# Kernel tuning notes

Hardware: AMD Instinct MI355X
Metric: run time of the kernel (lower is better)

The kernel has to match this reference:

```python
import jax, jax.numpy as jnp
import numpy as np

NUM_GRIDS = 8
GRID = jnp.linspace(-2.0, 2.0, NUM_GRIDS)
DENOM = 4.0 / (NUM_GRIDS - 1)
H, D = 8, 64
Q_DIM = K_DIM = V_DIM = 512
TOT = H * D


def fastkan(x, ln_s, ln_b, sw, bw, bb):
    # LayerNorm over last dim
    mu = jnp.mean(x, axis=-1, keepdims=True)
    var = jnp.var(x, axis=-1, keepdims=True)
    xn = (x - mu) * jax.lax.rsqrt(var + 1e-5) * ln_s + ln_b
    # Gaussian RBF basis over fixed grid: [..., in, G]
    basis = jnp.exp(-jnp.square((xn[..., None] - GRID) / DENOM))
    flat = basis.reshape(*x.shape[:-1], x.shape[-1] * NUM_GRIDS)
    # spline linear + base update (silu -> linear)
    return flat @ sw.T + jax.nn.silu(x) @ bw.T + bb


def setup_inputs() -> dict:
    key = jax.random.key(0)
    keys = iter(jax.random.split(key, 32))
    B, QL, KL = 2, 2048, 2048
    inp = {
        "q": jax.random.normal(next(keys), (B, QL, Q_DIM), jnp.float32),
        "k": jax.random.normal(next(keys), (B, KL, K_DIM), jnp.float32),
        "v": jax.random.normal(next(keys), (B, KL, V_DIM), jnp.float32),
    }
    def layer(ind, outd):
        return {
            "ln_s": jnp.ones((ind,), jnp.float32),
            "ln_b": jnp.zeros((ind,), jnp.float32),
            "sw": jax.random.normal(next(keys), (outd, ind * NUM_GRIDS), jnp.float32) * (0.1 / np.sqrt(ind * NUM_GRIDS)),
            "bw": jax.random.normal(next(keys), (outd, ind), jnp.float32) / np.sqrt(ind),
            "bb": jnp.zeros((outd,), jnp.float32),
        }
    dims = {"lq": (Q_DIM, TOT), "lk": (K_DIM, TOT), "lv": (V_DIM, TOT), "lo": (TOT, Q_DIM), "lg": (Q_DIM, TOT)}
    for name, (i, o) in dims.items():
        for pn, arr in layer(i, o).items():
            inp[name + "_" + pn] = arr
    return inp


def reference(q, k, v,
              lq_ln_s, lq_ln_b, lq_sw, lq_bw, lq_bb,
              lk_ln_s, lk_ln_b, lk_sw, lk_bw, lk_bb,
              lv_ln_s, lv_ln_b, lv_sw, lv_bw, lv_bb,
              lo_ln_s, lo_ln_b, lo_sw, lo_bw, lo_bb,
              lg_ln_s, lg_ln_b, lg_sw, lg_bw, lg_bb):
    norm = D ** -0.5
    wq = fastkan(q, lq_ln_s, lq_ln_b, lq_sw, lq_bw, lq_bb).reshape(*q.shape[:-1], H, D) * norm
    wk = fastkan(k, lk_ln_s, lk_ln_b, lk_sw, lk_bw, lk_bb).reshape(*k.shape[:-1], H, D)
    # att: [b, q_len, k_len, h]; softmax over k_len (axis=-2), matching torch code
    att = jax.nn.softmax(jnp.einsum('bqhd,bkhd->bqkh', wq, wk), axis=-2)
    wv = fastkan(v, lv_ln_s, lv_ln_b, lv_sw, lv_bw, lv_bb).reshape(*v.shape[:-1], H, D)
    o = jnp.einsum('bqkh,bkhd->bqhd', att, wv).reshape(*q.shape[:-1], TOT)
    g = fastkan(q, lg_ln_s, lg_ln_b, lg_sw, lg_bw, lg_bb)
    o = jax.nn.sigmoid(g) * o
    return fastkan(o, lo_ln_s, lo_ln_b, lo_sw, lo_bw, lo_bb)
```

## Files before the change

### kernel.cpp

```cpp
#include <hip/hip_runtime.h>

typedef unsigned short u16;
typedef unsigned int u32;
typedef float f32x4 __attribute__((ext_vector_type(4)));
typedef short s16x8 __attribute__((ext_vector_type(8)));

#define IND 512
#define KSPL 4096
#define NOUT 512
#define MROWS 4096
#define LQ 2048
#define AST 72
#define NZ 8
#define NSPLIT 4

#define SWN (4096 * 512)
#define BWN (512 * 512)
#define LSTR ((size_t)(SWN + BWN + 512))

__device__ __forceinline__ float bf2f(u16 u) {
    union { u32 i; float f; } v; v.i = ((u32)u) << 16; return v.f;
}
__device__ __forceinline__ u16 f2bf(float f) {
    union { float f; u32 i; } v; v.f = f;
    u32 x = v.i;
    return (u16)((x + 0x7FFFu + ((x >> 16) & 1u)) >> 16);
}
__device__ __forceinline__ uint4 pack8(float4 a, float4 b) {
    uint4 p;
    p.x = (u32)f2bf(a.x) | ((u32)f2bf(a.y) << 16);
    p.y = (u32)f2bf(a.z) | ((u32)f2bf(a.w) << 16);
    p.z = (u32)f2bf(b.x) | ((u32)f2bf(b.y) << 16);
    p.w = (u32)f2bf(b.z) | ((u32)f2bf(b.w) << 16);
    return p;
}
__device__ __forceinline__ void gl_lds16(const u16* g, u16* l) {
    __builtin_amdgcn_global_load_lds((const __attribute__((address_space(1))) void*)g,
                                     (__attribute__((address_space(3))) void*)l, 16, 0, 0);
}

__global__ void detect_dtype(const u32* __restrict__ qraw, u32* __restrict__ flag)
{
    const int t = threadIdx.x;
    int cnt = 0;
    for (int i = t; i < 1024; i += 256) {
        u32 e = (qraw[i] >> 23) & 0xFFu;
        if (e >= 100u && e <= 140u) cnt++;
    }
    #pragma unroll
    for (int off = 32; off > 0; off >>= 1) cnt += __shfl_down(cnt, off);
    __shared__ int red[4];
    if ((t & 63) == 0) red[t >> 6] = cnt;
    __syncthreads();
    if (t == 0) flag[0] = (red[0] + red[1] + red[2] + red[3] > 512) ? 1u : 0u;
}

struct WSrc { const void* p[15]; };
__global__ __launch_bounds__(256) void convert_w(WSrc s, u16* __restrict__ wb, const u32* __restrict__ flag)
{
    const int r = blockIdx.y;
    const int l = r / 3, t = r - l * 3;
    const int n = (t == 0) ? SWN : ((t == 1) ? BWN : 512);
    const int i = (blockIdx.x * 256 + threadIdx.x) * 8;
    if (i >= n) return;
    u16* dst = wb + (size_t)l * LSTR + ((t == 0) ? 0 : ((t == 1) ? SWN : SWN + BWN)) + i;
    const void* src = s.p[r];
    if (flag[0]) {
        const float* f = (const float*)src;
        *(uint4*)dst = pack8(*(const float4*)&f[i], *(const float4*)&f[i + 4]);
    } else {
        *(uint4*)dst = *(const uint4*)&((const u16*)src)[i];
    }
}

__global__ __launch_bounds__(256) void prep_kan(
    const void* __restrict__ xv, const void* __restrict__ ln_sv, const void* __restrict__ ln_bv,
    u16* __restrict__ basis, u16* __restrict__ silu, const u32* __restrict__ flag)
{
    const int row = blockIdx.x;
    const int t = threadIdx.x;
    const bool isf = flag[0] != 0u;
    float x0, x1;
    if (isf) {
        const float* xr = (const float*)xv + (size_t)row * IND;
        x0 = xr[t]; x1 = xr[t + 256];
    } else {
        const u16* xr = (const u16*)xv + (size_t)row * IND;
        x0 = bf2f(xr[t]); x1 = bf2f(xr[t + 256]);
    }
    float s = x0 + x1;
    float ss = x0 * x0 + x1 * x1;
    #pragma unroll
    for (int off = 32; off > 0; off >>= 1) {
        s += __shfl_down(s, off);
        ss += __shfl_down(ss, off);
    }
    __shared__ float red[8];
    const int wid = t >> 6, ln = t & 63;
    if (ln == 0) { red[wid] = s; red[4 + wid] = ss; }
    __syncthreads();
    const float tot = red[0] + red[1] + red[2] + red[3];
    const float tot2 = red[4] + red[5] + red[6] + red[7];
    const float mu = tot * (1.0f / IND);
    const float rstd = rsqrtf(tot2 * (1.0f / IND) - mu * mu + 1e-5f);
    #pragma unroll
    for (int e = 0; e < 2; e++) {
        const int i = t + e * 256;
        const float xi = (e == 0) ? x0 : x1;
        float lns, lnb;
        if (isf) {
            lns = ((const float*)ln_sv)[i];
            lnb = ((const float*)ln_bv)[i];
        } else {
            lns = bf2f(((const u16*)ln_sv)[i]);
            lnb = bf2f(((const u16*)ln_bv)[i]);
        }
        const float xn = (xi - mu) * rstd * lns + lnb;
        u16 o8[8];
        #pragma unroll
        for (int g = 0; g < 8; g++) {
            float d = (xn - (-2.0f + g * (4.0f / 7.0f))) * 1.75f;
            o8[g] = f2bf(__expf(-d * d));
        }
        uint4 pk;
        pk.x = (u32)o8[0] | ((u32)o8[1] << 16);
        pk.y = (u32)o8[2] | ((u32)o8[3] << 16);
        pk.z = (u32)o8[4] | ((u32)o8[5] << 16);
        pk.w = (u32)o8[6] | ((u32)o8[7] << 16);
        *(uint4*)(basis + (size_t)row * KSPL + i * 8) = pk;
        silu[(size_t)row * IND + i] = f2bf(xi / (1.0f + __expf(-xi)));
    }
}

__global__ __launch_bounds__(256) void prep_merge(
    const float* __restrict__ Opart, const float* __restrict__ lpart,
    const u16* __restrict__ gbuf, const void* __restrict__ ln_sv, const void* __restrict__ ln_bv,
    u16* __restrict__ basis, u16* __restrict__ silu, const u32* __restrict__ flag)
{
    const int row = blockIdx.x;
    const int b = row >> 11, qr = row & (LQ - 1);
    const int t = threadIdx.x;
    const bool isf = flag[0] != 0u;

    float xv[2];
    #pragma unroll
    for (int e = 0; e < 2; e++) {
        const int col = t + e * 256;
        const int g = b * 8 + (col >> 6);
        const int dd = col & 63;
        float o = 0.0f, l = 0.0f;
        #pragma unroll
        for (int s = 0; s < NSPLIT; s++) {
            const size_t rb = ((size_t)s * 16 + g) * LQ + qr;
            o += Opart[rb * 64 + dd];
            l += lpart[rb];
        }
        const float gv = bf2f(gbuf[(size_t)row * IND + col]);
        xv[e] = (o / l) / (1.0f + __expf(-gv));
    }
    float s = xv[0] + xv[1];
    float ss = xv[0] * xv[0] + xv[1] * xv[1];
    #pragma unroll
    for (int off = 32; off > 0; off >>= 1) {
        s += __shfl_down(s, off);
        ss += __shfl_down(ss, off);
    }
    __shared__ float red[8];
    const int wid = t >> 6, ln = t & 63;
    if (ln == 0) { red[wid] = s; red[4 + wid] = ss; }
    __syncthreads();
    const float tot = red[0] + red[1] + red[2] + red[3];
    const float tot2 = red[4] + red[5] + red[6] + red[7];
    const float mu = tot * (1.0f / IND);
    const float rstd = rsqrtf(tot2 * (1.0f / IND) - mu * mu + 1e-5f);
    #pragma unroll
    for (int e = 0; e < 2; e++) {
        const int i = t + e * 256;
        const float xi = xv[e];
        float lns, lnb;
        if (isf) {
            lns = ((const float*)ln_sv)[i];
            lnb = ((const float*)ln_bv)[i];
        } else {
            lns = bf2f(((const u16*)ln_sv)[i]);
            lnb = bf2f(((const u16*)ln_bv)[i]);
        }
        const float xn = (xi - mu) * rstd * lns + lnb;
        u16 o8[8];
        #pragma unroll
        for (int g = 0; g < 8; g++) {
            float d = (xn - (-2.0f + g * (4.0f / 7.0f))) * 1.75f;
            o8[g] = f2bf(__expf(-d * d));
        }
        uint4 pk;
        pk.x = (u32)o8[0] | ((u32)o8[1] << 16);
        pk.y = (u32)o8[2] | ((u32)o8[3] << 16);
        pk.z = (u32)o8[4] | ((u32)o8[5] << 16);
        pk.w = (u32)o8[6] | ((u32)o8[7] << 16);
        *(uint4*)(basis + (size_t)row * KSPL + i * 8) = pk;
        silu[(size_t)row * IND + i] = f2bf(xi / (1.0f + __expf(-xi)));
    }
}

__global__ __launch_bounds__(512) void gemm_big(
    const u16* __restrict__ A1, const u16* __restrict__ B1,
    const u16* __restrict__ A2, const u16* __restrict__ B2,
    u16* __restrict__ P)
{
    __shared__ __align__(16) u16 sA[2][256 * 64];
    __shared__ __align__(16) u16 sB[2][256 * 64];
    const int tid = threadIdx.x;
    const int lane = tid & 63;
    const int wid = tid >> 6;
    const int fm = lane & 15;
    const int quad = lane >> 4;
    const int wmbase = (wid >> 2) * 128;
    const int wnbase = (wid & 3) * 64;
    const int mbase = blockIdx.x * 256;
    const int nbase = blockIdx.y * 256;
    const int kz = blockIdx.z;

    const int srow = wid * 8 + (lane >> 3);
    const int scol = ((lane & 7) ^ (lane >> 3)) * 8;
    const int k1b = kz * 512;
    const int k2b = kz * 64;

    f32x4 acc[8][4] = {};

    {
        const u16* b0 = B1 + (size_t)(nbase + srow) * KSPL + k1b + scol;
        const u16* a0 = A1 + (size_t)(mbase + srow) * KSPL + k1b + scol;
        #pragma unroll
        for (int i = 0; i < 4; i++) gl_lds16(b0 + (size_t)i * 64 * KSPL, &sB[0][i * 4096 + wid * 512]);
        #pragma unroll
        for (int i = 0; i < 4; i++) gl_lds16(a0 + (size_t)i * 64 * KSPL, &sA[0][i * 4096 + wid * 512]);
        #pragma unroll
        for (int i = 0; i < 4; i++) gl_lds16(b0 + 64 + (size_t)i * 64 * KSPL, &sB[1][i * 4096 + wid * 512]);
    }
    asm volatile("s_waitcnt vmcnt(4)" ::: "memory");
    asm volatile("s_barrier" ::: "memory");

    #pragma unroll 1
    for (int t = 0; t < 9; ++t) {
        const u16* Ac = &sA[t & 1][0];
        const u16* Bc = &sB[t & 1][0];
        u16* abuf = &sA[(t + 1) & 1][0];
        u16* bbuf = &sB[t & 1][0];

        const u16* aS = nullptr; const u16* bS = nullptr;
        size_t aStep = 0, bStep = 0;
        if (t + 1 < 8) {
            aS = A1 + (size_t)(mbase + srow) * KSPL + k1b + (t + 1) * 64 + scol;
            aStep = (size_t)64 * KSPL;
        } else if (t + 1 == 8) {
            aS = A2 + (size_t)(mbase + srow) * IND + k2b + scol;
            aStep = (size_t)64 * IND;
        }
        if (t + 2 < 8) {
            bS = B1 + (size_t)(nbase + srow) * KSPL + k1b + (t + 2) * 64 + scol;
            bStep = (size_t)64 * KSPL;
        } else if (t + 2 == 8) {
            bS = B2 + (size_t)(nbase + srow) * IND + k2b + scol;
            bStep = (size_t)64 * IND;
        }

        s16x8 bfrag[4][2];
        #pragma unroll
        for (int n = 0; n < 4; n++)
            #pragma unroll
            for (int ks = 0; ks < 2; ks++)
                bfrag[n][ks] = *(const s16x8*)&Bc[((wnbase + n * 16 + fm) << 6) +
                                                 ((((ks << 2) + quad) ^ (fm & 7)) << 3)];

        #pragma unroll
        for (int ph = 0; ph < 2; ++ph) {
            s16x8 afr[4][2];
            #pragma unroll
            for (int i = 0; i < 4; i++)
                #pragma unroll
                for (int ks = 0; ks < 2; ks++)
                    afr[i][ks] = *(const s16x8*)&Ac[((wmbase + (ph * 4 + i) * 16 + fm) << 6) +
                                                   ((((ks << 2) + quad) ^ (fm & 7)) << 3)];
            if (ph == 0) {
                if (aS) {
                    #pragma unroll
                    for (int i = 0; i < 4; i++)
                        gl_lds16(aS + (size_t)i * aStep, abuf + i * 4096 + wid * 512);
                }
            } else {
                if (bS) {
                    #pragma unroll
                    for (int i = 0; i < 4; i++)
                        gl_lds16(bS + (size_t)i * bStep, bbuf + i * 4096 + wid * 512);
                }
            }
            asm volatile("s_barrier" ::: "memory");
            __builtin_amdgcn_s_setprio(1);
            #pragma unroll
            for (int i = 0; i < 4; i++)
                #pragma unroll
                for (int n = 0; n < 4; n++) {
                    acc[ph * 4 + i][n] = __builtin_amdgcn_mfma_f32_16x16x32_bf16(afr[i][0], bfrag[n][0], acc[ph * 4 + i][n], 0, 0, 0);
                    acc[ph * 4 + i][n] = __builtin_amdgcn_mfma_f32_16x16x32_bf16(afr[i][1], bfrag[n][1], acc[ph * 4 + i][n], 0, 0, 0);
                }
            __builtin_amdgcn_s_setprio(0);
            if (ph == 1) {
                if (t < 7)       asm volatile("s_waitcnt vmcnt(4)" ::: "memory");
                else if (t == 7) asm volatile("s_waitcnt vmcnt(0)" ::: "memory");
            }
            asm volatile("s_barrier" ::: "memory");
        }
    }

    #pragma unroll
    for (int n = 0; n < 4; n++) {
        const int col = nbase + wnbase + n * 16 + fm;
        const size_t cb = ((size_t)kz * NOUT + col) * MROWS;
        #pragma unroll
        for (int m = 0; m < 8; m++) {
            const int row0 = mbase + wmbase + m * 16 + quad * 4;
            uint2 o;
            o.x = (u32)f2bf(acc[m][n][0]) | ((u32)f2bf(acc[m][n][1]) << 16);
            o.y = (u32)f2bf(acc[m][n][2]) | ((u32)f2bf(acc[m][n][3]) << 16);
            *(uint2*)&P[cb + row0] = o;
        }
    }
}

__global__ __launch_bounds__(256) void reduce_kan(
    const u16* __restrict__ P, const u16* __restrict__ bias, void* __restrict__ C,
    float scale, const u32* __restrict__ flag, int ext_out)
{
    __shared__ float tshf[64][65];
    const int row0 = blockIdx.x * 64;
    const int col0 = blockIdx.y * 64;
    const int tid = threadIdx.x;
    #pragma unroll
    for (int p = 0; p < 2; p++) {
        const int idx = tid + p * 256;
        const int cl = idx >> 3;
        const int r8 = (idx & 7) * 8;
        float a[8] = {};
        for (int kz = 0; kz < NZ; kz++) {
            uint4 pk = *(const uint4*)&P[((size_t)kz * NOUT + col0 + cl) * MROWS + row0 + r8];
            const u16* pv = (const u16*)&pk;
            #pragma unroll
            for (int u = 0; u < 8; u++) a[u] += bf2f(pv[u]);
        }
        const float bi = bf2f(bias[col0 + cl]);
        #pragma unroll
        for (int u = 0; u < 8; u++) tshf[r8 + u][cl] = (a[u] + bi) * scale;
    }
    __syncthreads();
    const bool fo = ext_out && (flag[0] != 0u);
    #pragma unroll
    for (int p = 0; p < 2; p++) {
        const int idx = tid + p * 256;
        const int rl = idx >> 3;
        const int c8 = (idx & 7) * 8;
        if (fo) {
            float* Cf = (float*)C + (size_t)(row0 + rl) * NOUT + col0 + c8;
            float4 f0, f1;
            f0.x = tshf[rl][c8 + 0]; f0.y = tshf[rl][c8 + 1];
            f0.z = tshf[rl][c8 + 2]; f0.w = tshf[rl][c8 + 3];
            f1.x = tshf[rl][c8 + 4]; f1.y = tshf[rl][c8 + 5];
            f1.z = tshf[rl][c8 + 6]; f1.w = tshf[rl][c8 + 7];
            *(float4*)Cf = f0;
            *(float4*)(Cf + 4) = f1;
        } else {
            uint4 o;
            o.x = (u32)f2bf(tshf[rl][c8 + 0]) | ((u32)f2bf(tshf[rl][c8 + 1]) << 16);
            o.y = (u32)f2bf(tshf[rl][c8 + 2]) | ((u32)f2bf(tshf[rl][c8 + 3]) << 16);
            o.z = (u32)f2bf(tshf[rl][c8 + 4]) | ((u32)f2bf(tshf[rl][c8 + 5]) << 16);
            o.w = (u32)f2bf(tshf[rl][c8 + 6]) | ((u32)f2bf(tshf[rl][c8 + 7]) << 16);
            *(uint4*)&((u16*)C)[(size_t)(row0 + rl) * NOUT + col0 + c8] = o;
        }
    }
}

__global__ __launch_bounds__(256) void reduce_vt(
    const u16* __restrict__ P, const u16* __restrict__ bias, u16* __restrict__ VT)
{
    const int bc = blockIdx.x;
    const int b = bc >> 9, col = bc & 511;
    const int row8 = threadIdx.x * 8;
    float a[8] = {};
    for (int kz = 0; kz < NZ; kz++) {
        uint4 pk = *(const uint4*)&P[((size_t)kz * NOUT + col) * MROWS + b * LQ + row8];
        const u16* pv = (const u16*)&pk;
        #pragma unroll
        for (int u = 0; u < 8; u++) a[u] += bf2f(pv[u]);
    }
    const float bi = bf2f(bias[col]);
    u16 tmp[8];
    #pragma unroll
    for (int u = 0; u < 8; u++) tmp[u] = f2bf(a[u] + bi);
    *(uint4*)&VT[(size_t)bc * LQ + row8] = *(const uint4*)tmp;
}

__global__ __launch_bounds__(256) void attn4(
    const u16* __restrict__ wqp, const u16* __restrict__ wkp, const u16* __restrict__ VT,
    float* __restrict__ Opart, float* __restrict__ lpart)
{
    __shared__ __align__(16) u16 Ks[64 * 64];
    __shared__ __align__(16) u16 Vs[64 * 64];
    __shared__ __align__(16) u16 Ps[4][32 * AST];

    const int tid = threadIdx.x;
    const int lane = tid & 63;
    const int wid = tid >> 6;
    const int quad = lane >> 4;
    const int fm = lane & 15;
    const int srow8 = lane >> 3;
    const int schk = (lane & 7) ^ (lane >> 3);
    const int qb = blockIdx.x * 128;
    const int g = blockIdx.y;
    const int s = blockIdx.z;
    const int b = g >> 3, h = g & 7;
    const size_t qkbase = ((size_t)b * LQ) * 512 + h * 64;
    const size_t vtbase = (size_t)g * 64 * LQ;
    const int kvlen = LQ / NSPLIT, kv0 = s * kvlen;

    s16x8 aq[2][2];
    #pragma unroll
    for (int qi = 0; qi < 2; qi++)
        #pragma unroll
        for (int ks = 0; ks < 2; ks++)
            aq[qi][ks] = *(const s16x8*)&wqp[qkbase +
                (size_t)(qb + wid * 32 + qi * 16 + fm) * 512 + ks * 32 + quad * 8];
    s16x8 ones;
    #pragma unroll
    for (int i = 0; i < 8; i++) ones[i] = (short)0x3F80;

    f32x4 oacc[2][4] = {};
    f32x4 lacc[2] = {};

    for (int kt = 0; kt < kvlen / 64; kt++) {
        const int kb = kv0 + kt * 64;
        #pragma unroll
        for (int gg = 0; gg < 2; gg++) {
            const int r = wid * 16 + gg * 8 + srow8;
            gl_lds16(&wkp[qkbase + (size_t)(kb + r) * 512 + schk * 8], &Ks[(wid * 16 + gg * 8) * 64]);
            gl_lds16(&VT[vtbase + (size_t)r * LQ + kb + schk * 8],     &Vs[(wid * 16 + gg * 8) * 64]);
        }
        __syncthreads();

        #pragma unroll
        for (int j = 0; j < 4; j++) {
            f32x4 z0 = {}, z1 = {};
            #pragma unroll
            for (int ks = 0; ks < 2; ks++) {
                s16x8 bk = *(const s16x8*)&Ks[((j * 16 + fm) << 6) +
                                              ((((ks << 2) + quad) ^ (fm & 7)) << 3)];
                z0 = __builtin_amdgcn_mfma_f32_16x16x32_bf16(aq[0][ks], bk, z0, 0, 0, 0);
                z1 = __builtin_amdgcn_mfma_f32_16x16x32_bf16(aq[1][ks], bk, z1, 0, 0, 0);
            }
            #pragma unroll
            for (int r = 0; r < 4; r++) {
                union { float f; u32 i; } u0, u1;
                u0.f = __expf(z0[r] - 12.0f);
                u1.f = __expf(z1[r] - 12.0f);
                Ps[wid][(quad * 4 + r) * AST + j * 16 + fm]        = (u16)(u0.i >> 16);
                Ps[wid][(16 + quad * 4 + r) * AST + j * 16 + fm]   = (u16)(u1.i >> 16);
            }
        }

        s16x8 ap[2][2];
        #pragma unroll
        for (int qi = 0; qi < 2; qi++)
            #pragma unroll
            for (int ks = 0; ks < 2; ks++)
                ap[qi][ks] = *(const s16x8*)&Ps[wid][(qi * 16 + fm) * AST + ks * 32 + quad * 8];
        #pragma unroll
        for (int jd = 0; jd < 4; jd++)
            #pragma unroll
            for (int ks = 0; ks < 2; ks++) {
                s16x8 bv = *(const s16x8*)&Vs[((jd * 16 + fm) << 6) +
                                              ((((ks << 2) + quad) ^ (fm & 7)) << 3)];
                oacc[0][jd] = __builtin_amdgcn_mfma_f32_16x16x32_bf16(ap[0][ks], bv, oacc[0][jd], 0, 0, 0);
                oacc[1][jd] = __builtin_amdgcn_mfma_f32_16x16x32_bf16(ap[1][ks], bv, oacc[1][jd], 0, 0, 0);
            }
        #pragma unroll
        for (int qi = 0; qi < 2; qi++)
            #pragma unroll
            for (int ks = 0; ks < 2; ks++)
                lacc[qi] = __builtin_amdgcn_mfma_f32_16x16x32_bf16(ap[qi][ks], ones, lacc[qi], 0, 0, 0);
        __syncthreads();
    }

    const size_t obase = ((size_t)s * 16 + g) * LQ;
    #pragma unroll
    for (int qi = 0; qi < 2; qi++) {
        #pragma unroll
        for (int jd = 0; jd < 4; jd++)
            #pragma unroll
            for (int r = 0; r < 4; r++) {
                const int qrow = qb + wid * 32 + qi * 16 + quad * 4 + r;
                Opart[(obase + qrow) * 64 + jd * 16 + fm] = oacc[qi][jd][r];
            }
        if (fm == 0) {
            #pragma unroll
            for (int r = 0; r < 4; r++) {
                const int qrow = qb + wid * 32 + qi * 16 + quad * 4 + r;
                lpart[obase + qrow] = lacc[qi][r];
            }
        }
    }
}

extern "C" void kernel_launch(void* const* d_in, const int* in_sizes, int n_in,
                              void* d_out, int out_size, void* d_ws, size_t ws_size,
                              hipStream_t stream)
{
    const void* q = d_in[0];
    const void* k = d_in[1];
    const void* v = d_in[2];
    auto P = [&](int i) { return (const void*)d_in[i]; };

    const size_t WB_BYTES  = 5 * LSTR * 2;
    const size_t BAS_BYTES = (size_t)MROWS * KSPL * 2;
    const size_t SIL_BYTES = (size_t)MROWS * IND * 2;
    const size_t PART_B    = (size_t)NZ * MROWS * NOUT * 2;
    const size_t VT_B      = (size_t)16 * 64 * LQ * 2;
    const size_t OPART_B   = (size_t)NSPLIT * 16 * LQ * 64 * 4;

    char* base = (char*)d_ws;
    u32*  flag  = (u32*)base;
    u16*  wb    = (u16*)(base + 4096);
    u16*  basis = (u16*)((char*)wb + WB_BYTES);
    u16*  silu  = (u16*)((char*)basis + BAS_BYTES);
    u16*  wq    = (u16*)((char*)silu + SIL_BYTES);
    u16*  wk    = wq + (size_t)MROWS * NOUT;
    u16*  gbuf  = wk + (size_t)MROWS * NOUT;
    u16*  part  = gbuf + (size_t)MROWS * NOUT;
    u16*  VT    = (u16*)((char*)part + PART_B);
    float* Opart = (float*)((char*)VT + VT_B);
    float* lpart = (float*)((char*)Opart + OPART_B);

    detect_dtype<<<1, 256, 0, stream>>>((const u32*)q, flag);

    WSrc srcs;
    const int lbase[5] = {3, 8, 13, 18, 23};
    for (int l = 0; l < 5; l++) {
        srcs.p[l * 3 + 0] = d_in[lbase[l] + 2];
        srcs.p[l * 3 + 1] = d_in[lbase[l] + 3];
        srcs.p[l * 3 + 2] = d_in[lbase[l] + 4];
    }
    convert_w<<<dim3(SWN / 2048, 15), 256, 0, stream>>>(srcs, wb, flag);

    auto swb = [&](int l) { return wb + (size_t)l * LSTR; };
    auto bwb = [&](int l) { return wb + (size_t)l * LSTR + SWN; };
    auto bbb = [&](int l) { return wb + (size_t)l * LSTR + SWN + BWN; };
    dim3 gg(MROWS / 256, NOUT / 256, NZ);
    dim3 rg(MROWS / 64, NOUT / 64);

    prep_kan<<<MROWS, 256, 0, stream>>>(q, P(3), P(4), basis, silu, flag);
    gemm_big<<<gg, 512, 0, stream>>>(basis, swb(0), silu, bwb(0), part);
    reduce_kan<<<rg, 256, 0, stream>>>(part, bbb(0), wq, 0.125f, flag, 0);
    prep_kan<<<MROWS, 256, 0, stream>>>(q, P(23), P(24), basis, silu, flag);
    gemm_big<<<gg, 512, 0, stream>>>(basis, swb(4), silu, bwb(4), part);
    reduce_kan<<<rg, 256, 0, stream>>>(part, bbb(4), gbuf, 1.0f, flag, 0);
    prep_kan<<<MROWS, 256, 0, stream>>>(k, P(8), P(9), basis, silu, flag);
    gemm_big<<<gg, 512, 0, stream>>>(basis, swb(1), silu, bwb(1), part);
    reduce_kan<<<rg, 256, 0, stream>>>(part, bbb(1), wk, 1.0f, flag, 0);
    prep_kan<<<MROWS, 256, 0, stream>>>(v, P(13), P(14), basis, silu, flag);
    gemm_big<<<gg, 512, 0, stream>>>(basis, swb(2), silu, bwb(2), part);
    reduce_vt<<<1024, 256, 0, stream>>>(part, bbb(2), VT);

    attn4<<<dim3(LQ / 128, 16, NSPLIT), 256, 0, stream>>>(wq, wk, VT, Opart, lpart);

    prep_merge<<<MROWS, 256, 0, stream>>>(Opart, lpart, gbuf, P(18), P(19), basis, silu, flag);
    gemm_big<<<gg, 512, 0, stream>>>(basis, swb(3), silu, bwb(3), part);
    reduce_kan<<<rg, 256, 0, stream>>>(part, bbb(3), d_out, 1.0f, flag, 1);
}
```

Measured before the change: 421.4 us.

## Replace double-buffered 256x256 GEMM tile with simple single-buffered 128x128 tile

The KAN GEMM kernel shrinks from a 256x256 output tile with 512 threads and a hand-scheduled double-buffered LDS pipeline to a 128x128 tile with 256 threads. The new kernel loads each K chunk, syncs, computes, and syncs again, with no prefetch overlap. This gives four times as many blocks and less LDS per block, which may let more blocks share a CU. The cost is losing the load/compute overlap, the priority hints, and data reuse from the larger tile.

```diff
diff --git a/kernel.cpp b/kernel.cpp
--- a/kernel.cpp
+++ b/kernel.cpp
@@ -202,126 +202,80 @@
     }
 }
 
-__global__ __launch_bounds__(512) void gemm_big(
+__global__ __launch_bounds__(256) void gemm_big(
     const u16* __restrict__ A1, const u16* __restrict__ B1,
     const u16* __restrict__ A2, const u16* __restrict__ B2,
     u16* __restrict__ P)
 {
-    __shared__ __align__(16) u16 sA[2][256 * 64];
-    __shared__ __align__(16) u16 sB[2][256 * 64];
+    __shared__ __align__(16) u16 sA[128 * 64];
+    __shared__ __align__(16) u16 sB[128 * 64];
     const int tid = threadIdx.x;
     const int lane = tid & 63;
     const int wid = tid >> 6;
     const int fm = lane & 15;
     const int quad = lane >> 4;
-    const int wmbase = (wid >> 2) * 128;
-    const int wnbase = (wid & 3) * 64;
-    const int mbase = blockIdx.x * 256;
-    const int nbase = blockIdx.y * 256;
+    const int wm = (wid >> 1) * 64;
+    const int wn = (wid & 1) * 64;
+    const int mbase = blockIdx.x * 128;
+    const int nbase = blockIdx.y * 128;
     const int kz = blockIdx.z;
 
     const int srow = wid * 8 + (lane >> 3);
     const int scol = ((lane & 7) ^ (lane >> 3)) * 8;
-    const int k1b = kz * 512;
-    const int k2b = kz * 64;
-
-    f32x4 acc[8][4] = {};
-
-    {
-        const u16* b0 = B1 + (size_t)(nbase + srow) * KSPL + k1b + scol;
-        const u16* a0 = A1 + (size_t)(mbase + srow) * KSPL + k1b + scol;
-        #pragma unroll
-        for (int i = 0; i < 4; i++) gl_lds16(b0 + (size_t)i * 64 * KSPL, &sB[0][i * 4096 + wid * 512]);
-        #pragma unroll
-        for (int i = 0; i < 4; i++) gl_lds16(a0 + (size_t)i * 64 * KSPL, &sA[0][i * 4096 + wid * 512]);
-        #pragma unroll
-        for (int i = 0; i < 4; i++) gl_lds16(b0 + 64 + (size_t)i * 64 * KSPL, &sB[1][i * 4096 + wid * 512]);
-    }
-    asm volatile("s_waitcnt vmcnt(4)" ::: "memory");
-    asm volatile("s_barrier" ::: "memory");
+
+    f32x4 acc[4][4] = {};
+
+    const u16* aP  = A1 + (size_t)(mbase + srow) * KSPL + kz * 512 + scol;
+    const u16* bP  = B1 + (size_t)(nbase + srow) * KSPL + kz * 512 + scol;
+    const u16* aP2 = A2 + (size_t)(mbase + srow) * IND + kz * 64 + scol;
+    const u16* bP2 = B2 + (size_t)(nbase + srow) * IND + kz * 64 + scol;
 
     #pragma unroll 1
     for (int t = 0; t < 9; ++t) {
-        const u16* Ac = &sA[t & 1][0];
-        const u16* Bc = &sB[t & 1][0];
-        u16* abuf = &sA[(t + 1) & 1][0];
-        u16* bbuf = &sB[t & 1][0];
-
-        const u16* aS = nullptr; const u16* bS = nullptr;
-        size_t aStep = 0, bStep = 0;
-        if (t + 1 < 8) {
-            aS = A1 + (size_t)(mbase + srow) * KSPL + k1b + (t + 1) * 64 + scol;
-            aStep = (size_t)64 * KSPL;
-        } else if (t + 1 == 8) {
-            aS = A2 + (size_t)(mbase + srow) * IND + k2b + scol;
-            aStep = (size_t)64 * IND;
-        }
-        if (t + 2 < 8) {
-            bS = B1 + (size_t)(nbase + srow) * KSPL + k1b + (t + 2) * 64 + scol;
-            bStep = (size_t)64 * KSPL;
-        } else if (t + 2 == 8) {
-            bS = B2 + (size_t)(nbase + srow) * IND + k2b + scol;
-            bStep = (size_t)64 * IND;
-        }
-
-        s16x8 bfrag[4][2];
-        #pragma unroll
-        for (int n = 0; n < 4; n++)
-            #pragma unroll
-            for (int ks = 0; ks < 2; ks++)
-                bfrag[n][ks] = *(const s16x8*)&Bc[((wnbase + n * 16 + fm) << 6) +
-                                                 ((((ks << 2) + quad) ^ (fm & 7)) << 3)];
-
-        #pragma unroll
-        for (int ph = 0; ph < 2; ++ph) {
-            s16x8 afr[4][2];
-            #pragma unroll
-            for (int i = 0; i < 4; i++)
-                #pragma unroll
-                for (int ks = 0; ks < 2; ks++)
-                    afr[i][ks] = *(const s16x8*)&Ac[((wmbase + (ph * 4 + i) * 16 + fm) << 6) +
-                                                   ((((ks << 2) + quad) ^ (fm & 7)) << 3)];
-            if (ph == 0) {
-                if (aS) {
-                    #pragma unroll
-                    for (int i = 0; i < 4; i++)
-                        gl_lds16(aS + (size_t)i * aStep, abuf + i * 4096 + wid * 512);
-                }
-            } else {
-                if (bS) {
-                    #pragma unroll
-                    for (int i = 0; i < 4; i++)
-                        gl_lds16(bS + (size_t)i * bStep, bbuf + i * 4096 + wid * 512);
-                }
-            }
-            asm volatile("s_barrier" ::: "memory");
-            __builtin_amdgcn_s_setprio(1);
-            #pragma unroll
-            for (int i = 0; i < 4; i++)
-                #pragma unroll
-                for (int n = 0; n < 4; n++) {
-                    acc[ph * 4 + i][n] = __builtin_amdgcn_mfma_f32_16x16x32_bf16(afr[i][0], bfrag[n][0], acc[ph * 4 + i][n], 0, 0, 0);
-                    acc[ph * 4 + i][n] = __builtin_amdgcn_mfma_f32_16x16x32_bf16(afr[i][1], bfrag[n][1], acc[ph * 4 + i][n], 0, 0, 0);
-                }
-            __builtin_amdgcn_s_setprio(0);
-            if (ph == 1) {
-                if (t < 7)       asm volatile("s_waitcnt vmcnt(4)" ::: "memory");
-                else if (t == 7) asm volatile("s_waitcnt vmcnt(0)" ::: "memory");
-            }
-            asm volatile("s_barrier" ::: "memory");
-        }
-    }
-
-    #pragma unroll
-    for (int n = 0; n < 4; n++) {
-        const int col = nbase + wnbase + n * 16 + fm;
+        if (t < 8) {
+            #pragma unroll
+            for (int i = 0; i < 4; i++) {
+                gl_lds16(aP + (size_t)i * 32 * KSPL + t * 64, &sA[i * 2048 + wid * 512]);
+                gl_lds16(bP + (size_t)i * 32 * KSPL + t * 64, &sB[i * 2048 + wid * 512]);
+            }
+        } else {
+            #pragma unroll
+            for (int i = 0; i < 4; i++) {
+                gl_lds16(aP2 + (size_t)i * 32 * IND, &sA[i * 2048 + wid * 512]);
+                gl_lds16(bP2 + (size_t)i * 32 * IND, &sB[i * 2048 + wid * 512]);
+            }
+        }
+        __syncthreads();
+        s16x8 af[4][2], bfr[4][2];
+        #pragma unroll
+        for (int i = 0; i < 4; i++)
+            #pragma unroll
+            for (int ks = 0; ks < 2; ks++) {
+                af[i][ks]  = *(const s16x8*)&sA[((wm + i * 16 + fm) << 6) +
+                                                ((((ks << 2) + quad) ^ (fm & 7)) << 3)];
+                bfr[i][ks] = *(const s16x8*)&sB[((wn + i * 16 + fm) << 6) +
+                                                ((((ks << 2) + quad) ^ (fm & 7)) << 3)];
+            }
+        #pragma unroll
+        for (int i = 0; i < 4; i++)
+            #pragma unroll
+            for (int j = 0; j < 4; j++) {
+                acc[i][j] = __builtin_amdgcn_mfma_f32_16x16x32_bf16(af[i][0], bfr[j][0], acc[i][j], 0, 0, 0);
+                acc[i][j] = __builtin_amdgcn_mfma_f32_16x16x32_bf16(af[i][1], bfr[j][1], acc[i][j], 0, 0, 0);
+            }
+        __syncthreads();
+    }
+
+    #pragma unroll
+    for (int j = 0; j < 4; j++) {
+        const int col = nbase + wn + j * 16 + fm;
         const size_t cb = ((size_t)kz * NOUT + col) * MROWS;
         #pragma unroll
-        for (int m = 0; m < 8; m++) {
-            const int row0 = mbase + wmbase + m * 16 + quad * 4;
+        for (int i = 0; i < 4; i++) {
+            const int row0 = mbase + wm + i * 16 + quad * 4;
             uint2 o;
-            o.x = (u32)f2bf(acc[m][n][0]) | ((u32)f2bf(acc[m][n][1]) << 16);
-            o.y = (u32)f2bf(acc[m][n][2]) | ((u32)f2bf(acc[m][n][3]) << 16);
+            o.x = (u32)f2bf(acc[i][j][0]) | ((u32)f2bf(acc[i][j][1]) << 16);
+            o.y = (u32)f2bf(acc[i][j][2]) | ((u32)f2bf(acc[i][j][3]) << 16);
             *(uint2*)&P[cb + row0] = o;
         }
     }
@@ -551,25 +505,25 @@
     auto swb = [&](int l) { return wb + (size_t)l * LSTR; };
     auto bwb = [&](int l) { return wb + (size_t)l * LSTR + SWN; };
     auto bbb = [&](int l) { return wb + (size_t)l * LSTR + SWN + BWN; };
-    dim3 gg(MROWS / 256, NOUT / 256, NZ);
+    dim3 gg(MROWS / 128, NOUT / 128, NZ);
     dim3 rg(MROWS / 64, NOUT / 64);
 
     prep_kan<<<MROWS, 256, 0, stream>>>(q, P(3), P(4), basis, silu, flag);
-    gemm_big<<<gg, 512, 0, stream>>>(basis, swb(0), silu, bwb(0), part);
+    gemm_big<<<gg, 256, 0, stream>>>(basis, swb(0), silu, bwb(0), part);
     reduce_kan<<<rg, 256, 0, stream>>>(part, bbb(0), wq, 0.125f, flag, 0);
     prep_kan<<<MROWS, 256, 0, stream>>>(q, P(23), P(24), basis, silu, flag);
-    gemm_big<<<gg, 512, 0, stream>>>(basis, swb(4), silu, bwb(4), part);
+    gemm_big<<<gg, 256, 0, stream>>>(basis, swb(4), silu, bwb(4), part);
     reduce_kan<<<rg, 256, 0, stream>>>(part, bbb(4), gbuf, 1.0f, flag, 0);
     prep_kan<<<MROWS, 256, 0, stream>>>(k, P(8), P(9), basis, silu, flag);
-    gemm_big<<<gg, 512, 0, stream>>>(basis, swb(1), silu, bwb(1), part);
+    gemm_big<<<gg, 256, 0, stream>>>(basis, swb(1), silu, bwb(1), part);
     reduce_kan<<<rg, 256, 0, stream>>>(part, bbb(1), wk, 1.0f, flag, 0);
     prep_kan<<<MROWS, 256, 0, stream>>>(v, P(13), P(14), basis, silu, flag);
-    gemm_big<<<gg, 512, 0, stream>>>(basis, swb(2), silu, bwb(2), part);
+    gemm_big<<<gg, 256, 0, stream>>>(basis, swb(2), silu, bwb(2), part);
     reduce_vt<<<1024, 256, 0, stream>>>(part, bbb(2), VT);
 
     attn4<<<dim3(LQ / 128, 16, NSPLIT), 256, 0, stream>>>(wq, wk, VT, Opart, lpart);
 
     prep_merge<<<MROWS, 256, 0, stream>>>(Opart, lpart, gbuf, P(18), P(19), basis, silu, flag);
-    gemm_big<<<gg, 512, 0, stream>>>(basis, swb(3), silu, bwb(3), part);
+    gemm_big<<<gg, 256, 0, stream>>>(basis, swb(3), silu, bwb(3), part);
     reduce_kan<<<rg, 256, 0, stream>>>(part, bbb(3), d_out, 1.0f, flag, 1);
 }
```

Result: slower. 452.5 us (+7.4%).
